# Kernel tuning notes

Measured on AMD Instinct MI355X. Metric: run time of the kernel, lower is better.

## Reference

```python
import jax, jax.numpy as jnp
import numpy as np

EPS = 1e-20
K = 3  # kernel_size


def _patches(x, k=K):
    # emulates KernelChannels.kernel_channels / F.unfold with stride=1, padding=0, dilation=1
    # x: (B, C, H, W) -> (B, C, k*k, H-k+1, W-k+1); depth index kk = i*k + j maps to offset (i, j)
    Ho = x.shape[2] - k + 1
    Wo = x.shape[3] - k + 1
    return jnp.stack([x[:, :, i:i + Ho, j:j + Wo] for i in range(k) for j in range(k)], axis=2)


def setup_inputs() -> dict:
    key = jax.random.key(0)
    ks = jax.random.split(key, 13)
    B, C, O, H, W = 2, 32, 32, 256, 512
    Ho, Wo = H - K + 1, W - K + 1
    d = jax.random.uniform(ks[0], (B, C, H, W), dtype=jnp.float32)
    cd = jax.random.uniform(ks[1], (B, C, H, W), dtype=jnp.float32)
    s = jax.random.uniform(ks[2], (B, C, H, W), dtype=jnp.float32)
    cs = jax.random.uniform(ks[3], (B, C, H, W), dtype=jnp.float32)
    gx = jax.random.normal(ks[4], (B, C, H, W), dtype=jnp.float32)
    cgx = jax.random.uniform(ks[5], (B, C, H, W), dtype=jnp.float32)
    gy = jax.random.normal(ks[6], (B, C, H, W), dtype=jnp.float32)
    cgy = jax.random.uniform(ks[7], (B, C, H, W), dtype=jnp.float32)
    s_prod_roll = jax.random.uniform(ks[8], (B, C, K * K, Ho, Wo), dtype=jnp.float32)
    # learned parameters (raw; EnforcePos applies softplus inside forward)
    w_prop = jax.random.normal(ks[9], (1, 1, 1, 1), dtype=jnp.float32) * 0.1
    spatial_weight = jax.random.normal(ks[10], (C, 1, K * K, 1, 1), dtype=jnp.float32) * 0.1
    channel_weight = jax.random.normal(ks[11], (O, C, 1, 1), dtype=jnp.float32) * 0.1
    bias = jax.random.normal(ks[12], (1, O, 1, 1), dtype=jnp.float32) * 0.01
    return {"d": d, "cd": cd, "s": s, "cs": cs, "gx": gx, "cgx": cgx, "gy": gy,
            "cgy": cgy, "s_prod_roll": s_prod_roll, "w_prop": w_prop,
            "spatial_weight": spatial_weight, "channel_weight": channel_weight, "bias": bias}


def reference(d, cd, s, cs, gx, cgx, gy, cgy, s_prod_roll,
              w_prop, spatial_weight, channel_weight, bias):
    stride = 1
    # roll-based vertical neighbor gather with confidence zeroing at borders
    d_up = jnp.roll(d, 1, axis=2)
    cd_up = jnp.roll(cd, 1, axis=2).at[:, :, 0, :].set(0.0)
    s_up = jnp.roll(s, 1, axis=2)
    d_down = jnp.roll(d, -1, axis=2)
    cd_down = jnp.roll(cd, -1, axis=2).at[:, :, -1, :].set(0.0)
    s_down = jnp.roll(s, -1, axis=2)

    cgy_from_ds = s * s_up * s_down * cd_up * cd_up  # faithful to source (cd_up twice)
    height = (cd_up * d_up + cd_down * d_down) / (cd_up + cd_down + EPS)
    gy_from_ds = (d_down - d_up) / 2.0 / (height + EPS)

    w = jax.nn.softplus(w_prop)[0, 0, 0, 0]  # EnforcePos on w_prop
    gy_f = (w * cgy * gy + cgy_from_ds * gy_from_ds) / (w * cgy + cgy_from_ds + EPS)
    cgy_f = (w * cgy + cgy_from_ds) / (w + 1.0)

    # kernel-channel expansion (B, C, k*k, Ho, Wo)
    gy_roll = _patches(gy_f)
    cgy_roll = _patches(cgy_f)
    cgy_prop = cgy_roll * s_prod_roll

    # grouped conv3d with (C,1,k*k,1,1) kernel, groups=C == per-channel weighted sum over k*k
    sw = jax.nn.softplus(spatial_weight)[:, 0, :, 0, 0]  # (C, k*k)
    nom = jnp.einsum('bckhw,ck->bchw', cgy_prop * gy_roll, sw)
    den = jnp.einsum('bckhw,ck->bchw', cgy_prop, sw)
    gy_sp = nom / (den + EPS)
    cgy_sp = den / jnp.sum(sw)

    # 1x1 conv2d across channels (groups=1)
    cw = jax.nn.softplus(channel_weight)[:, :, 0, 0]  # (O, C)
    nom2 = jnp.einsum('bchw,oc->bohw', cgy_sp * gy_sp, cw)
    den2 = jnp.einsum('bchw,oc->bohw', cgy_sp, cw)
    gy_out = nom2 / (den2 + EPS) + bias
    cgy_out = den2 / jnp.sum(cw)
    return (gy_out * stride, cgy_out / stride / stride)
```

## Files before the change

### kernel.cpp

```cpp
#include <hip/hip_runtime.h>

#define EPSF 1e-20f

typedef float v2f __attribute__((ext_vector_type(2)));

constexpr int B_ = 2, C_ = 32, O_ = 32, H_ = 256, W_ = 512;
constexpr int HO = 254, WO = 510;
constexpr int HW  = H_ * W_;
constexpr int PLO = HO * WO;
constexpr int OUT1 = B_ * O_ * PLO;
constexpr int IMG  = B_ * C_ * HW;
constexpr int WT2  = 64;

__device__ __forceinline__ float sp_(float x) { return log1pf(expf(x)); }
__device__ __forceinline__ float rcp_(float x) { return __builtin_amdgcn_rcpf(x); }

__device__ __forceinline__ unsigned bfpack(float g, float c) {
  unsigned ug = __float_as_uint(g);
  unsigned uc = __float_as_uint(c);
  ug = ug + 0x7FFFu + ((ug >> 16) & 1u);
  uc = uc + 0x7FFFu + ((uc >> 16) & 1u);
  return (ug >> 16) | (uc & 0xFFFF0000u);
}
__device__ __forceinline__ float bf_lo(unsigned u) { return __uint_as_float(u << 16); }
__device__ __forceinline__ float bf_hi(unsigned u) { return __uint_as_float(u & 0xFFFF0000u); }

__global__ __launch_bounds__(256) void k_setup(const float* __restrict__ w_prop,
                                               const float* __restrict__ spw,
                                               const float* __restrict__ chw,
                                               float* __restrict__ params) {
  __shared__ float red[256];
  int t = threadIdx.x;
  float l1 = 0.f;
  for (int i = t; i < 288; i += 256) { float v = sp_(spw[i]); params[16 + i] = v; l1 += v; }
  red[t] = l1; __syncthreads();
  for (int k = 128; k > 0; k >>= 1) { if (t < k) red[t] += red[t + k]; __syncthreads(); }
  float SW = red[0]; __syncthreads();
  float l2 = 0.f;
  for (int i = t; i < 1024; i += 256) {
    int o = i >> 5, c = i & 31;
    float v = sp_(chw[o * C_ + c]);
    params[304 + c * O_ + o] = v;
    l2 += v;
  }
  red[t] = l2; __syncthreads();
  for (int k = 128; k > 0; k >>= 1) { if (t < k) red[t] += red[t + k]; __syncthreads(); }
  if (t == 0) { params[0] = sp_(w_prop[0]); params[1] = SW; params[2] = red[0]; }
}

__global__ __launch_bounds__(256) void k1_gyf(const float* __restrict__ d,
                                              const float* __restrict__ cd,
                                              const float* __restrict__ s,
                                              const float* __restrict__ gy,
                                              const float* __restrict__ cgy,
                                              const float* __restrict__ params,
                                              unsigned* __restrict__ I) {
  const float w      = params[0];
  const float inv_w1 = rcp_(w + 1.0f);
  const int idx = blockIdx.x * 256 + threadIdx.x;
  const long i4 = (long)idx * 4;
  const int h = (int)((i4 >> 9) & (H_ - 1));
  const long up = (h == 0)      ? i4 + (long)(H_ - 1) * W_ : i4 - W_;
  const long dn = (h == H_ - 1) ? i4 - (long)(H_ - 1) * W_ : i4 + W_;

  float4 duv = *(const float4*)(d + up);
  float4 ddv = *(const float4*)(d + dn);
  float4 sv  = *(const float4*)(s + i4);
  float4 suv = *(const float4*)(s + up);
  float4 sdv = *(const float4*)(s + dn);
  float4 cduv = (h == 0)      ? make_float4(0.f, 0.f, 0.f, 0.f) : *(const float4*)(cd + up);
  float4 cddv = (h == H_ - 1) ? make_float4(0.f, 0.f, 0.f, 0.f) : *(const float4*)(cd + dn);
  float4 gyv  = *(const float4*)(gy + i4);
  float4 cgyv = *(const float4*)(cgy + i4);

  const float* pdu = (const float*)&duv;  const float* pdd = (const float*)&ddv;
  const float* ps  = (const float*)&sv;   const float* psu = (const float*)&suv;
  const float* psd = (const float*)&sdv;  const float* pcu = (const float*)&cduv;
  const float* pcd = (const float*)&cddv; const float* pg  = (const float*)&gyv;
  const float* pc  = (const float*)&cgyv;

  uint4 o;
  unsigned* po = (unsigned*)&o;
#pragma unroll
  for (int j = 0; j < 4; ++j) {
    const float cu = pcu[j], cdn = pcd[j];
    const float cfd = ps[j] * psu[j] * psd[j] * cu * cu;
    const float height = (cu * pdu[j] + cdn * pdd[j]) * rcp_(cu + cdn + EPSF);
    const float gfd = (pdd[j] - pdu[j]) * 0.5f * rcp_(height + EPSF);
    const float a = w * pc[j];
    const float vg = (a * pg[j] + cfd * gfd) * rcp_(a + cfd + EPSF);
    const float vc = (a + cfd) * inv_w1;
    po[j] = bfpack(vg, vc);
  }
  *(uint4*)(I + i4) = o;
}

__global__ __launch_bounds__(256) void k2_fused(const unsigned* __restrict__ I,
                                                const float* __restrict__ spr,
                                                const float* __restrict__ params,
                                                const float* __restrict__ bias,
                                                float* __restrict__ out) {
  __shared__ float sw_s[288];
  __shared__ v2f AB[C_][WT2 + 2];

  const int b   = blockIdx.z;
  const int ho  = blockIdx.y;
  const int wo0 = blockIdx.x * WT2;
  const int t   = threadIdx.x;

  for (int i = t; i < 288; i += 256) sw_s[i] = params[16 + i];
  const float invSW = rcp_(params[1]);
  const float invCW = rcp_(params[2]);
  __syncthreads();

  const int pp = t & 31;
  const int cg = t >> 5;
  const int wo  = wo0 + 2 * pp;
  const int wos = (wo <= WO - 2) ? wo : (WO - 2);

#pragma unroll
  for (int ci = 0; ci < 4; ++ci) {
    const int c = cg * 4 + ci;
    const unsigned* Ip = I + (b * C_ + c) * HW + ho * W_ + wos;
    uint2 r0a = *(const uint2*)(Ip);
    uint2 r0b = *(const uint2*)(Ip + 2);
    uint2 r1a = *(const uint2*)(Ip + W_);
    uint2 r1b = *(const uint2*)(Ip + W_ + 2);
    uint2 r2a = *(const uint2*)(Ip + 2 * W_);
    uint2 r2b = *(const uint2*)(Ip + 2 * W_ + 2);

    const float* sp = spr + (long)(b * C_ + c) * 9 * PLO + ho * WO + wos;
    v2f spv[9];
#pragma unroll
    for (int k = 0; k < 9; ++k) spv[k] = *(const v2f*)(sp + (long)k * PLO);

    unsigned urow[3][4] = {{r0a.x, r0a.y, r0b.x, r0b.y},
                           {r1a.x, r1a.y, r1b.x, r1b.y},
                           {r2a.x, r2a.y, r2b.x, r2b.y}};
    float gf[3][4], cf[3][4];
#pragma unroll
    for (int i = 0; i < 3; ++i)
#pragma unroll
      for (int j = 0; j < 4; ++j) { gf[i][j] = bf_lo(urow[i][j]); cf[i][j] = bf_hi(urow[i][j]); }

#pragma unroll
    for (int u = 0; u < 2; ++u) {
      float nom = 0.f, den = 0.f;
#pragma unroll
      for (int i = 0; i < 3; ++i) {
#pragma unroll
        for (int j = 0; j < 3; ++j) {
          const float cp = cf[i][u + j] * spv[i * 3 + j][u] * sw_s[c * 9 + i * 3 + j];
          nom += cp * gf[i][u + j];
          den += cp;
        }
      }
      const float gy_sp  = nom * rcp_(den + EPSF);
      const float cgy_sp = den * invSW;
      AB[c][2 * pp + u] = (v2f){gy_sp * cgy_sp, cgy_sp};
    }
  }
  __syncthreads();

  const int px  = t & 63;
  const int og  = __builtin_amdgcn_readfirstlane(t >> 6);
  const int wob = wo0 + px;

  v2f ab[C_];
#pragma unroll
  for (int c = 0; c < C_; ++c) ab[c] = AB[c][px];

  const float* cwT = params + 304;
  v2f acc[8];
#pragma unroll
  for (int oj = 0; oj < 8; ++oj) acc[oj] = (v2f){0.f, 0.f};
#pragma unroll
  for (int c = 0; c < C_; ++c) {
#pragma unroll
    for (int oj = 0; oj < 8; ++oj)
      acc[oj] += ab[c] * cwT[c * O_ + og * 8 + oj];
  }

  if (wob < WO) {
    const int obase = b * O_ * PLO + ho * WO + wob;
#pragma unroll
    for (int oj = 0; oj < 8; ++oj) {
      const int o = og * 8 + oj;
      out[obase + o * PLO]        = acc[oj].x * rcp_(acc[oj].y + EPSF) + bias[o];
      out[OUT1 + obase + o * PLO] = acc[oj].y * invCW;
    }
  }
}

extern "C" void kernel_launch(void* const* d_in, const int* in_sizes, int n_in,
                              void* d_out, int out_size, void* d_ws, size_t ws_size,
                              hipStream_t stream) {
  const float* d      = (const float*)d_in[0];
  const float* cd     = (const float*)d_in[1];
  const float* s      = (const float*)d_in[2];
  const float* gy     = (const float*)d_in[6];
  const float* cgy    = (const float*)d_in[7];
  const float* spr    = (const float*)d_in[8];
  const float* w_prop = (const float*)d_in[9];
  const float* spw    = (const float*)d_in[10];
  const float* chw    = (const float*)d_in[11];
  const float* bias   = (const float*)d_in[12];
  float* out = (float*)d_out;

  float* params = (float*)d_ws;
  unsigned* I   = (unsigned*)d_ws + 4096;

  k_setup<<<1, 256, 0, stream>>>(w_prop, spw, chw, params);

  k1_gyf<<<IMG / 4 / 256, 256, 0, stream>>>(d, cd, s, gy, cgy, params, I);

  dim3 g2(8, HO, B_);
  k2_fused<<<g2, 256, 0, stream>>>(I, spr, params, bias, out);
}
```

Measured before the change: 149.0 us.

## Widen k2 tile to 128 pixels with double-buffered channel loads and transposed LDS

The fused second kernel now covers 128 output pixels per block, with each wave handling 8 channels. Loads for the next channel are issued before the current channel is computed, using two register buffers. The LDS intermediate is transposed to pixel-major with padding so the channel-mix stage reads vec4s, and each thread accumulates two pixels so the weight loads are shared. Spatial weights are read straight from params instead of being staged in LDS, which removes one barrier. The cost is higher register pressure (launch bounds of 4 blocks) and half as many blocks in the grid.

```diff
diff --git a/kernel.cpp b/kernel.cpp
--- a/kernel.cpp
+++ b/kernel.cpp
@@ -3,6 +3,7 @@
 #define EPSF 1e-20f
 
 typedef float v2f __attribute__((ext_vector_type(2)));
+typedef float v4f __attribute__((ext_vector_type(4)));
 
 constexpr int B_ = 2, C_ = 32, O_ = 32, H_ = 256, W_ = 512;
 constexpr int HO = 254, WO = 510;
@@ -10,7 +11,8 @@
 constexpr int PLO = HO * WO;
 constexpr int OUT1 = B_ * O_ * PLO;
 constexpr int IMG  = B_ * C_ * HW;
-constexpr int WT2  = 64;
+constexpr int WT2  = 128;
+constexpr int ABS_ = 68;
 
 __device__ __forceinline__ float sp_(float x) { return log1pf(expf(x)); }
 __device__ __forceinline__ float rcp_(float x) { return __builtin_amdgcn_rcpf(x); }
@@ -95,99 +97,128 @@
   *(uint4*)(I + i4) = o;
 }
 
-__global__ __launch_bounds__(256) void k2_fused(const unsigned* __restrict__ I,
-                                                const float* __restrict__ spr,
-                                                const float* __restrict__ params,
-                                                const float* __restrict__ bias,
-                                                float* __restrict__ out) {
-  __shared__ float sw_s[288];
-  __shared__ v2f AB[C_][WT2 + 2];
+struct Ch { uint2 r[3][2]; v2f sp[9]; };
+
+__global__ __launch_bounds__(256, 4) void k2_fused(const unsigned* __restrict__ I,
+                                                   const float* __restrict__ spr,
+                                                   const float* __restrict__ params,
+                                                   const float* __restrict__ bias,
+                                                   float* __restrict__ out) {
+  __shared__ float AB[WT2][ABS_];
 
   const int b   = blockIdx.z;
   const int ho  = blockIdx.y;
   const int wo0 = blockIdx.x * WT2;
   const int t   = threadIdx.x;
 
-  for (int i = t; i < 288; i += 256) sw_s[i] = params[16 + i];
   const float invSW = rcp_(params[1]);
   const float invCW = rcp_(params[2]);
-  __syncthreads();
-
-  const int pp = t & 31;
-  const int cg = t >> 5;
+
+  const int pp  = t & 63;
+  const int cg  = __builtin_amdgcn_readfirstlane(t >> 6);
   const int wo  = wo0 + 2 * pp;
   const int wos = (wo <= WO - 2) ? wo : (WO - 2);
-
-#pragma unroll
-  for (int ci = 0; ci < 4; ++ci) {
-    const int c = cg * 4 + ci;
-    const unsigned* Ip = I + (b * C_ + c) * HW + ho * W_ + wos;
-    uint2 r0a = *(const uint2*)(Ip);
-    uint2 r0b = *(const uint2*)(Ip + 2);
-    uint2 r1a = *(const uint2*)(Ip + W_);
-    uint2 r1b = *(const uint2*)(Ip + W_ + 2);
-    uint2 r2a = *(const uint2*)(Ip + 2 * W_);
-    uint2 r2b = *(const uint2*)(Ip + 2 * W_ + 2);
-
-    const float* sp = spr + (long)(b * C_ + c) * 9 * PLO + ho * WO + wos;
-    v2f spv[9];
-#pragma unroll
-    for (int k = 0; k < 9; ++k) spv[k] = *(const v2f*)(sp + (long)k * PLO);
-
-    unsigned urow[3][4] = {{r0a.x, r0a.y, r0b.x, r0b.y},
-                           {r1a.x, r1a.y, r1b.x, r1b.y},
-                           {r2a.x, r2a.y, r2b.x, r2b.y}};
+  const int c0  = cg * 8;
+
+  const unsigned* Ibase = I + (b * C_ + c0) * HW + ho * W_ + wos;
+  const float*    Sbase = spr + (long)(b * C_ + c0) * 9 * PLO + ho * WO + wos;
+
+  auto loadc = [&](int ci, Ch& L) {
+    const unsigned* Ip = Ibase + ci * HW;
+#pragma unroll
+    for (int i = 0; i < 3; ++i) {
+      L.r[i][0] = *(const uint2*)(Ip + i * W_);
+      L.r[i][1] = *(const uint2*)(Ip + i * W_ + 2);
+    }
+    const float* sp = Sbase + (long)ci * 9 * PLO;
+#pragma unroll
+    for (int k = 0; k < 9; ++k) L.sp[k] = *(const v2f*)(sp + (long)k * PLO);
+  };
+
+  auto computec = [&](int ci, const Ch& L) {
     float gf[3][4], cf[3][4];
 #pragma unroll
-    for (int i = 0; i < 3; ++i)
-#pragma unroll
-      for (int j = 0; j < 4; ++j) { gf[i][j] = bf_lo(urow[i][j]); cf[i][j] = bf_hi(urow[i][j]); }
-
+    for (int i = 0; i < 3; ++i) {
+      const unsigned uu[4] = {L.r[i][0].x, L.r[i][0].y, L.r[i][1].x, L.r[i][1].y};
+#pragma unroll
+      for (int j = 0; j < 4; ++j) { gf[i][j] = bf_lo(uu[j]); cf[i][j] = bf_hi(uu[j]); }
+    }
+    const float* swc = params + 16 + (c0 + ci) * 9;
 #pragma unroll
     for (int u = 0; u < 2; ++u) {
       float nom = 0.f, den = 0.f;
 #pragma unroll
-      for (int i = 0; i < 3; ++i) {
+      for (int i = 0; i < 3; ++i)
 #pragma unroll
         for (int j = 0; j < 3; ++j) {
-          const float cp = cf[i][u + j] * spv[i * 3 + j][u] * sw_s[c * 9 + i * 3 + j];
+          const float cp = cf[i][u + j] * L.sp[i * 3 + j][u] * swc[i * 3 + j];
           nom += cp * gf[i][u + j];
           den += cp;
         }
-      }
       const float gy_sp  = nom * rcp_(den + EPSF);
       const float cgy_sp = den * invSW;
-      AB[c][2 * pp + u] = (v2f){gy_sp * cgy_sp, cgy_sp};
-    }
+      *(v2f*)&AB[2 * pp + u][2 * (c0 + ci)] = (v2f){gy_sp * cgy_sp, cgy_sp};
+    }
+  };
+
+  {
+    Ch Ca, Cb;
+    loadc(0, Ca);
+    loadc(1, Cb);
+    computec(0, Ca);
+    loadc(2, Ca);
+    computec(1, Cb);
+    loadc(3, Cb);
+    computec(2, Ca);
+    loadc(4, Ca);
+    computec(3, Cb);
+    loadc(5, Cb);
+    computec(4, Ca);
+    loadc(6, Ca);
+    computec(5, Cb);
+    loadc(7, Cb);
+    computec(6, Ca);
+    computec(7, Cb);
   }
   __syncthreads();
 
-  const int px  = t & 63;
-  const int og  = __builtin_amdgcn_readfirstlane(t >> 6);
-  const int wob = wo0 + px;
-
-  v2f ab[C_];
-#pragma unroll
-  for (int c = 0; c < C_; ++c) ab[c] = AB[c][px];
-
+  const int px0 = t & 63;
+  const int px1 = px0 + 64;
+  const int ogr = __builtin_amdgcn_readfirstlane(t >> 6);
   const float* cwT = params + 304;
-  v2f acc[8];
-#pragma unroll
-  for (int oj = 0; oj < 8; ++oj) acc[oj] = (v2f){0.f, 0.f};
-#pragma unroll
-  for (int c = 0; c < C_; ++c) {
-#pragma unroll
-    for (int oj = 0; oj < 8; ++oj)
-      acc[oj] += ab[c] * cwT[c * O_ + og * 8 + oj];
-  }
-
-  if (wob < WO) {
-    const int obase = b * O_ * PLO + ho * WO + wob;
+
+  v2f acc0[8], acc1[8];
+#pragma unroll
+  for (int oj = 0; oj < 8; ++oj) { acc0[oj] = (v2f){0.f, 0.f}; acc1[oj] = (v2f){0.f, 0.f}; }
+
+#pragma unroll
+  for (int c2 = 0; c2 < C_; c2 += 2) {
+    const v4f a0 = *(const v4f*)&AB[px0][2 * c2];
+    const v4f a1 = *(const v4f*)&AB[px1][2 * c2];
+    const float* w0 = cwT + c2 * O_ + ogr * 8;
+    const float* w1 = w0 + O_;
+    const v2f g00 = (v2f){a0.x, a0.y}, g01 = (v2f){a0.z, a0.w};
+    const v2f g10 = (v2f){a1.x, a1.y}, g11 = (v2f){a1.z, a1.w};
 #pragma unroll
     for (int oj = 0; oj < 8; ++oj) {
-      const int o = og * 8 + oj;
-      out[obase + o * PLO]        = acc[oj].x * rcp_(acc[oj].y + EPSF) + bias[o];
-      out[OUT1 + obase + o * PLO] = acc[oj].y * invCW;
+      acc0[oj] += g00 * w0[oj];
+      acc0[oj] += g01 * w1[oj];
+      acc1[oj] += g10 * w0[oj];
+      acc1[oj] += g11 * w1[oj];
+    }
+  }
+
+  const int  wob1 = wo0 + px1;
+  const long ob   = (long)b * O_ * PLO + (long)ho * WO + wo0;
+#pragma unroll
+  for (int oj = 0; oj < 8; ++oj) {
+    const int o = ogr * 8 + oj;
+    const float bv = bias[o];
+    out[ob + (long)o * PLO + px0]        = acc0[oj].x * rcp_(acc0[oj].y + EPSF) + bv;
+    out[OUT1 + ob + (long)o * PLO + px0] = acc0[oj].y * invCW;
+    if (wob1 < WO) {
+      out[ob + (long)o * PLO + px1]        = acc1[oj].x * rcp_(acc1[oj].y + EPSF) + bv;
+      out[OUT1 + ob + (long)o * PLO + px1] = acc1[oj].y * invCW;
     }
   }
 }
@@ -214,6 +245,6 @@
 
   k1_gyf<<<IMG / 4 / 256, 256, 0, stream>>>(d, cd, s, gy, cgy, params, I);
 
-  dim3 g2(8, HO, B_);
+  dim3 g2(WT2 == 128 ? 4 : 8, HO, B_);
   k2_fused<<<g2, 256, 0, stream>>>(I, spr, params, bias, out);
 }
```

Result: slower. 199.3 us (+33.8%).
